# Performance work log

Hardware: AMD Instinct MI355X
Metric: run time of the kernel (lower is better)

## Reference

```python
import jax, jax.numpy as jnp
import numpy as np

N = 128 * 128          # hardcoded in the original forward: x.view(1, 1, 128*128)
SCORE_LIMIT = int(0.5 * N)   # int(score_limit * num_inputs) = 8192
K = 7                  # odd kernel_size, padding = K // 2 = 3


def setup_inputs() -> dict:
    key = jax.random.key(0)
    k1, k2 = jax.random.split(key)
    x = jax.random.normal(k1, (N,), dtype=jnp.float32)
    # Conv1d(1, 1, K, bias=False) weight, flattened to a length-K taps vector
    conv_w = jax.random.normal(k2, (K,), dtype=jnp.float32) * 0.1
    return {"x": x, "conv_w": conv_w}


def reference(x, conv_w):
    # torch Conv1d is cross-correlation with 'same' padding (K odd):
    # y[i] = sum_j w[j] * x[i + j - K//2]. jnp.convolve flips the kernel,
    # so pass conv_w reversed to get cross-correlation.
    y = jnp.convolve(x, conv_w[::-1], mode="same")
    attention_score = jax.nn.sigmoid(y)                     # [N]
    attention_index = jnp.argsort(attention_score)          # ascending, [N]
    keep = attention_index[:SCORE_LIMIT]                    # lowest-score indices kept (as in source)
    simple_score = attention_score[keep] + 1.0              # [SCORE_LIMIT]
    # zeros everywhere, scatter rescaled values at kept indices
    new_x = jnp.zeros_like(x).at[keep].set(x[keep] * simple_score)
    return new_x, attention_score
```

## Files before the change

### kernel.cpp

```cpp
#include <hip/hip_runtime.h>
#include <math.h>

#define N 16384
#define LIMIT 8192
#define NT 1024
#define G 16
#define EPT 16


__device__ __forceinline__ unsigned long long make_key(float s, int i) {
    return ((unsigned long long)__float_as_uint(s) << 14) | (unsigned int)i;
}

template <int W, int WIDTH>
__device__ __forceinline__ void scan_select(unsigned int* tot,
                                            unsigned int* partial,
                                            unsigned long long* prefix_sh,
                                            unsigned int* r_sh,
                                            unsigned int* m_sh) {
    const int tid = threadIdx.x;
    const unsigned int r = *r_sh;
    if (tid < 256) {
        unsigned int p = 0;
#pragma unroll
        for (int q = 0; q < W / 4; ++q) {
            uint4 v = ((const uint4*)tot)[tid * (W / 4) + q];
            p += v.x + v.y + v.z + v.w;
        }
        partial[tid] = p;
    }
    __syncthreads();
    if (tid < 64) {
        unsigned int p0 = partial[4*tid+0], p1 = partial[4*tid+1],
                     p2 = partial[4*tid+2], p3 = partial[4*tid+3];
        const unsigned int g4 = p0 + p1 + p2 + p3;
        unsigned int incl = g4;
#pragma unroll
        for (int d = 1; d < 64; d <<= 1) {
            unsigned int up = __shfl_up(incl, d, 64);
            if (tid >= d) incl += up;
        }
        unsigned long long ball = __ballot(incl > r);
        int L = __ffsll((long long)ball) - 1;
        if (tid == L) {
            unsigned int cum = incl - g4;
            unsigned int pp[4] = {p0, p1, p2, p3};
            int grp = -1;
#pragma unroll
            for (int k = 0; k < 4; ++k)
                if (grp < 0) { if (cum + pp[k] > r) grp = 4*L + k; else cum += pp[k]; }
            unsigned int c[W];
#pragma unroll
            for (int q = 0; q < W / 4; ++q) {
                uint4 v = ((const uint4*)tot)[grp * (W / 4) + q];
                c[4*q+0] = v.x; c[4*q+1] = v.y; c[4*q+2] = v.z; c[4*q+3] = v.w;
            }
            int b = -1; unsigned int mm = 0;
#pragma unroll
            for (int k = 0; k < W; ++k)
                if (b < 0) {
                    if (cum + c[k] > r) { b = grp * W + k; mm = c[k]; }
                    else cum += c[k];
                }
            *r_sh = r - cum;
            *m_sh = mm;
            *prefix_sh = (*prefix_sh << WIDTH) | (unsigned long long)b;
        }
    }
    __syncthreads();
}

__global__ __launch_bounds__(NT)
void mono_kernel(const float* __restrict__ x, const float* __restrict__ w,
                 float* __restrict__ out) {
    __shared__ __attribute__((aligned(16))) unsigned int hist0[4096];
    __shared__ __attribute__((aligned(16))) unsigned int tot[1024];
    __shared__ __attribute__((aligned(16))) unsigned int hist1[4096];
    __shared__ __attribute__((aligned(16))) unsigned int partial[256];
    __shared__ unsigned long long prefix_sh;
    __shared__ unsigned int r_sh, m_sh, ccnt, tlow_sh;
    __shared__ unsigned int cand[64];

    const int tid = threadIdx.x;
    const int blk = blockIdx.x;
    const int base = tid * EPT;

    float wv[7];
#pragma unroll
    for (int t = 0; t < 7; ++t) wv[t] = w[t];

    float win[EPT + 6];
    const float4* xv = (const float4*)(x + base);
#pragma unroll
    for (int q = 0; q < 4; ++q) {
        float4 v = xv[q];
        win[3 + 4*q + 0] = v.x; win[3 + 4*q + 1] = v.y;
        win[3 + 4*q + 2] = v.z; win[3 + 4*q + 3] = v.w;
    }
#pragma unroll
    for (int t = 0; t < 3; ++t) {
        int jl = base - 3 + t;
        win[t] = (jl >= 0) ? x[jl] : 0.f;
        int jr = base + EPT + t;
        win[EPT + 3 + t] = (jr < N) ? x[jr] : 0.f;
    }

    hist0[tid] = 0; hist0[tid+1024] = 0; hist0[tid+2048] = 0; hist0[tid+3072] = 0;
    hist1[tid] = 0; hist1[tid+1024] = 0; hist1[tid+2048] = 0; hist1[tid+3072] = 0;
    tot[tid] = 0;
    if (tid == 0) { prefix_sh = 0ULL; r_sh = LIMIT - 1; ccnt = 0; }

    float s[EPT];
#pragma unroll
    for (int k = 0; k < EPT; ++k) {
        float acc = 0.f;
#pragma unroll
        for (int t = 0; t < 7; ++t)
            acc = __fadd_rn(acc, __fmul_rn(win[k + t], wv[t]));
        s[k] = 1.f / (1.f + expf(-acc));
    }

    if ((tid >> 6) == blk) {
        float4* so = (float4*)(out + N + base);
#pragma unroll
        for (int q = 0; q < 4; ++q)
            so[q] = make_float4(s[4*q], s[4*q+1], s[4*q+2], s[4*q+3]);
    }
    __syncthreads();

    const int slot = tid & 3;
#pragma unroll
    for (int k = 0; k < EPT; ++k) {
        unsigned int bin = __float_as_uint(s[k]) >> 20;
        atomicAdd(&hist0[(bin << 2) | slot], 1u);
    }
    __syncthreads();
    {
        uint4 v = ((const uint4*)hist0)[tid];
        tot[tid] = v.x + v.y + v.z + v.w;
    }
    __syncthreads();
    scan_select<4, 10>(tot, partial, &prefix_sh, &r_sh, &m_sh);

    {
        const unsigned long long pref = prefix_sh;
#pragma unroll
        for (int k = 0; k < EPT; ++k) {
            unsigned long long key = make_key(s[k], base + k);
            if ((key >> 34) == pref)
                atomicAdd(&hist1[(unsigned int)(key >> 22) & 4095u], 1u);
        }
    }
    __syncthreads();
    scan_select<16, 12>(hist1, partial, &prefix_sh, &r_sh, &m_sh);

    unsigned long long T;
    const unsigned int M = m_sh;
    const unsigned int r1 = r_sh;
    if (M <= 64u) {
        const unsigned long long pref = prefix_sh;
#pragma unroll
        for (int k = 0; k < EPT; ++k) {
            unsigned long long key = make_key(s[k], base + k);
            if ((key >> 22) == pref) {
                unsigned int pos = atomicAdd(&ccnt, 1u);
                cand[pos] = (unsigned int)(key & 0x3FFFFFu);
            }
        }
        __syncthreads();
        if (tid < 64) {
            unsigned int v = (tid < (int)M) ? cand[tid] : 0xFFFFFFFFu;
            unsigned int cnt = 0;
#pragma unroll
            for (int i = 0; i < 64; ++i) {
                unsigned int vi = __shfl(v, i, 64);
                cnt += (vi < v) ? 1u : 0u;
            }
            if (tid < (int)M && cnt == r1) tlow_sh = v;
        }
        __syncthreads();
        T = (prefix_sh << 22) | (unsigned long long)tlow_sh;
    } else {
        hist1[tid] = 0; hist1[tid + 1024] = 0;
        __syncthreads();
        {
            const unsigned long long pref = prefix_sh;
#pragma unroll
            for (int k = 0; k < EPT; ++k) {
                unsigned long long key = make_key(s[k], base + k);
                if ((key >> 22) == pref)
                    atomicAdd(&hist1[(unsigned int)(key >> 11) & 2047u], 1u);
            }
        }
        __syncthreads();
        scan_select<8, 11>(hist1, partial, &prefix_sh, &r_sh, &m_sh);
        hist1[tid] = 0; hist1[tid + 1024] = 0;
        __syncthreads();
        {
            const unsigned long long pref = prefix_sh;
#pragma unroll
            for (int k = 0; k < EPT; ++k) {
                unsigned long long key = make_key(s[k], base + k);
                if ((key >> 11) == pref)
                    atomicAdd(&hist1[(unsigned int)key & 2047u], 1u);
            }
        }
        __syncthreads();
        scan_select<8, 11>(hist1, partial, &prefix_sh, &r_sh, &m_sh);
        T = prefix_sh;
    }

    if ((tid >> 6) == blk) {
        float4* no = (float4*)(out + base);
#pragma unroll
        for (int q = 0; q < 4; ++q) {
            float4 v; float* vp = &v.x;
#pragma unroll
            for (int e = 0; e < 4; ++e) {
                int k = 4*q + e;
                unsigned long long key = make_key(s[k], base + k);
                vp[e] = (key <= T) ? __fmul_rn(win[3 + k], __fadd_rn(s[k], 1.0f)) : 0.f;
            }
            no[q] = v;
        }
    }
}

extern "C" void kernel_launch(void* const* d_in, const int* in_sizes, int n_in,
                              void* d_out, int out_size, void* d_ws, size_t ws_size,
                              hipStream_t stream) {
    const float* x = (const float*)d_in[0];
    const float* w = (const float*)d_in[1];
    float* out = (float*)d_out;
    mono_kernel<<<G, NT, 0, stream>>>(x, w, out);
}
```

Before: 65.50 us.

## Replace two-level radix select with single fine histogram over sigmoid range

```diff
diff --git a/kernel.cpp b/kernel.cpp
--- a/kernel.cpp
+++ b/kernel.cpp
@@ -6,20 +6,24 @@
 #define NT 1024
 #define G 16
 #define EPT 16
+#define LO 0x3E800000u
+#define HI 0x3F800000u
+#define BSH 11
+#define NB 8192
 
 
 __device__ __forceinline__ unsigned long long make_key(float s, int i) {
     return ((unsigned long long)__float_as_uint(s) << 14) | (unsigned int)i;
 }
 
-template <int W, int WIDTH>
-__device__ __forceinline__ void scan_select(unsigned int* tot,
+template <int W>
+__device__ __forceinline__ void scan_select(const unsigned int* tot,
                                             unsigned int* partial,
-                                            unsigned long long* prefix_sh,
-                                            unsigned int* r_sh,
+                                            unsigned int r,
+                                            unsigned int* b_sh,
+                                            unsigned int* r_out,
                                             unsigned int* m_sh) {
     const int tid = threadIdx.x;
-    const unsigned int r = *r_sh;
     if (tid < 256) {
         unsigned int p = 0;
 #pragma unroll
@@ -41,30 +45,34 @@
             if (tid >= d) incl += up;
         }
         unsigned long long ball = __ballot(incl > r);
-        int L = __ffsll((long long)ball) - 1;
-        if (tid == L) {
-            unsigned int cum = incl - g4;
-            unsigned int pp[4] = {p0, p1, p2, p3};
-            int grp = -1;
-#pragma unroll
-            for (int k = 0; k < 4; ++k)
-                if (grp < 0) { if (cum + pp[k] > r) grp = 4*L + k; else cum += pp[k]; }
-            unsigned int c[W];
-#pragma unroll
-            for (int q = 0; q < W / 4; ++q) {
-                uint4 v = ((const uint4*)tot)[grp * (W / 4) + q];
-                c[4*q+0] = v.x; c[4*q+1] = v.y; c[4*q+2] = v.z; c[4*q+3] = v.w;
-            }
-            int b = -1; unsigned int mm = 0;
-#pragma unroll
-            for (int k = 0; k < W; ++k)
-                if (b < 0) {
-                    if (cum + c[k] > r) { b = grp * W + k; mm = c[k]; }
-                    else cum += c[k];
+        if (ball == 0ULL) {
+            if (tid == 0) *m_sh = 0xFFFFFFFFu;
+        } else {
+            int L = __ffsll((long long)ball) - 1;
+            if (tid == L) {
+                unsigned int cum = incl - g4;
+                unsigned int pp[4] = {p0, p1, p2, p3};
+                int grp = -1;
+#pragma unroll
+                for (int k = 0; k < 4; ++k)
+                    if (grp < 0) { if (cum + pp[k] > r) grp = 4*L + k; else cum += pp[k]; }
+                unsigned int c[W];
+#pragma unroll
+                for (int q = 0; q < W / 4; ++q) {
+                    uint4 v = ((const uint4*)tot)[grp * (W / 4) + q];
+                    c[4*q+0] = v.x; c[4*q+1] = v.y; c[4*q+2] = v.z; c[4*q+3] = v.w;
                 }
-            *r_sh = r - cum;
-            *m_sh = mm;
-            *prefix_sh = (*prefix_sh << WIDTH) | (unsigned long long)b;
+                int b = -1; unsigned int mm = 0;
+#pragma unroll
+                for (int k = 0; k < W; ++k)
+                    if (b < 0) {
+                        if (cum + c[k] > r) { b = grp * W + k; mm = c[k]; }
+                        else cum += c[k];
+                    }
+                *r_out = r - cum;
+                *m_sh = mm;
+                *b_sh = (unsigned int)b;
+            }
         }
     }
     __syncthreads();
@@ -73,13 +81,10 @@
 __global__ __launch_bounds__(NT)
 void mono_kernel(const float* __restrict__ x, const float* __restrict__ w,
                  float* __restrict__ out) {
-    __shared__ __attribute__((aligned(16))) unsigned int hist0[4096];
-    __shared__ __attribute__((aligned(16))) unsigned int tot[1024];
-    __shared__ __attribute__((aligned(16))) unsigned int hist1[4096];
+    __shared__ __attribute__((aligned(16))) unsigned int hist[NB];
     __shared__ __attribute__((aligned(16))) unsigned int partial[256];
-    __shared__ unsigned long long prefix_sh;
-    __shared__ unsigned int r_sh, m_sh, ccnt, tlow_sh;
     __shared__ unsigned int cand[64];
+    __shared__ unsigned int b_sh, r1_sh, m_sh, below_sh, ccnt, tlow_sh;
 
     const int tid = threadIdx.x;
     const int blk = blockIdx.x;
@@ -105,10 +110,9 @@
         win[EPT + 3 + t] = (jr < N) ? x[jr] : 0.f;
     }
 
-    hist0[tid] = 0; hist0[tid+1024] = 0; hist0[tid+2048] = 0; hist0[tid+3072] = 0;
-    hist1[tid] = 0; hist1[tid+1024] = 0; hist1[tid+2048] = 0; hist1[tid+3072] = 0;
-    tot[tid] = 0;
-    if (tid == 0) { prefix_sh = 0ULL; r_sh = LIMIT - 1; ccnt = 0; }
+    ((uint4*)hist)[tid] = make_uint4(0,0,0,0);
+    ((uint4*)hist)[tid + 1024] = make_uint4(0,0,0,0);
+    if (tid == 0) { below_sh = 0; ccnt = 0; }
 
     float s[EPT];
 #pragma unroll
@@ -128,86 +132,67 @@
     }
     __syncthreads();
 
-    const int slot = tid & 3;
+    unsigned int cnt = 0;
 #pragma unroll
     for (int k = 0; k < EPT; ++k) {
-        unsigned int bin = __float_as_uint(s[k]) >> 20;
-        atomicAdd(&hist0[(bin << 2) | slot], 1u);
-    }
-    __syncthreads();
-    {
-        uint4 v = ((const uint4*)hist0)[tid];
-        tot[tid] = v.x + v.y + v.z + v.w;
-    }
-    __syncthreads();
-    scan_select<4, 10>(tot, partial, &prefix_sh, &r_sh, &m_sh);
-
-    {
-        const unsigned long long pref = prefix_sh;
+        const unsigned int u = __float_as_uint(s[k]);
+        if (u < LO) ++cnt;
+        else if (u < HI) atomicAdd(&hist[(u - LO) >> BSH], 1u);
+    }
+#pragma unroll
+    for (int d = 32; d > 0; d >>= 1) cnt += __shfl_down(cnt, d, 64);
+    if ((tid & 63) == 0 && cnt) atomicAdd(&below_sh, cnt);
+    __syncthreads();
+
+    const unsigned int r0 = (LIMIT - 1) - below_sh;
+    scan_select<32>(hist, partial, r0, &b_sh, &r1_sh, &m_sh);
+    const unsigned int M = m_sh;
+
+    unsigned long long T;
+    if (M <= 64u) {
+        const unsigned int b = b_sh, r1 = r1_sh;
 #pragma unroll
         for (int k = 0; k < EPT; ++k) {
-            unsigned long long key = make_key(s[k], base + k);
-            if ((key >> 34) == pref)
-                atomicAdd(&hist1[(unsigned int)(key >> 22) & 4095u], 1u);
-        }
-    }
-    __syncthreads();
-    scan_select<16, 12>(hist1, partial, &prefix_sh, &r_sh, &m_sh);
-
-    unsigned long long T;
-    const unsigned int M = m_sh;
-    const unsigned int r1 = r_sh;
-    if (M <= 64u) {
-        const unsigned long long pref = prefix_sh;
-#pragma unroll
-        for (int k = 0; k < EPT; ++k) {
-            unsigned long long key = make_key(s[k], base + k);
-            if ((key >> 22) == pref) {
+            const unsigned int u = __float_as_uint(s[k]);
+            if (u >= LO && u < HI && ((u - LO) >> BSH) == b) {
                 unsigned int pos = atomicAdd(&ccnt, 1u);
-                cand[pos] = (unsigned int)(key & 0x3FFFFFu);
+                cand[pos] = ((u & 0x7FFu) << 14) | (unsigned int)(base + k);
             }
         }
         __syncthreads();
         if (tid < 64) {
             unsigned int v = (tid < (int)M) ? cand[tid] : 0xFFFFFFFFu;
-            unsigned int cnt = 0;
+            unsigned int c = 0;
 #pragma unroll
             for (int i = 0; i < 64; ++i) {
                 unsigned int vi = __shfl(v, i, 64);
-                cnt += (vi < v) ? 1u : 0u;
-            }
-            if (tid < (int)M && cnt == r1) tlow_sh = v;
+                c += (vi < v) ? 1u : 0u;
+            }
+            if (tid < (int)M && c == r1) tlow_sh = v;
         }
         __syncthreads();
-        T = (prefix_sh << 22) | (unsigned long long)tlow_sh;
+        const unsigned int R = tlow_sh;
+        const unsigned int ustar = LO + (b << BSH) + (R >> 14);
+        T = ((unsigned long long)ustar << 14) | (unsigned long long)(R & 0x3FFFu);
     } else {
-        hist1[tid] = 0; hist1[tid + 1024] = 0;
-        __syncthreads();
-        {
-            const unsigned long long pref = prefix_sh;
+        unsigned long long prefix = 0ULL;
+        unsigned int r2 = LIMIT - 1;
+        for (int p = 0; p < 4; ++p) {
+            const int shift = 33 - 11 * p;
+            hist[tid] = 0; hist[tid + 1024] = 0;
+            __syncthreads();
 #pragma unroll
             for (int k = 0; k < EPT; ++k) {
                 unsigned long long key = make_key(s[k], base + k);
-                if ((key >> 22) == pref)
-                    atomicAdd(&hist1[(unsigned int)(key >> 11) & 2047u], 1u);
-            }
-        }
-        __syncthreads();
-        scan_select<8, 11>(hist1, partial, &prefix_sh, &r_sh, &m_sh);
-        hist1[tid] = 0; hist1[tid + 1024] = 0;
-        __syncthreads();
-        {
-            const unsigned long long pref = prefix_sh;
-#pragma unroll
-            for (int k = 0; k < EPT; ++k) {
-                unsigned long long key = make_key(s[k], base + k);
-                if ((key >> 11) == pref)
-                    atomicAdd(&hist1[(unsigned int)key & 2047u], 1u);
-            }
-        }
-        __syncthreads();
-        scan_select<8, 11>(hist1, partial, &prefix_sh, &r_sh, &m_sh);
-        T = prefix_sh;
+                if ((key >> (shift + 11)) == prefix)
+                    atomicAdd(&hist[(unsigned int)(key >> shift) & 2047u], 1u);
+            }
+            __syncthreads();
+            scan_select<8>(hist, partial, r2, &b_sh, &r1_sh, &m_sh);
+            prefix = (prefix << 11) | (unsigned long long)b_sh;
+            r2 = r1_sh;
+        }
+        T = prefix;
     }
 
     if ((tid >> 6) == blk) {
```

After: 65.48 us. No clear change (-0.0%).
